# Performance work log

Measured on AMD Instinct MI355X. Metric: run time of the kernel, lower is better.

## Reference

```python
import jax, jax.numpy as jnp
import numpy as np

D_MODEL = 1024
D_STATE = 8
EXPAND = 2
EPS = 1e-5


def setup_inputs() -> dict:
    key = jax.random.key(0)
    ks = jax.random.split(key, 8)
    d_inner = D_MODEL * EXPAND
    x = jax.random.normal(ks[0], (2, 128, 196, D_MODEL), dtype=jnp.float32)
    # Linear params (torch convention: W [out, in], y = x @ W.T + b)
    W_proj = jax.random.normal(ks[1], (d_inner, D_MODEL), dtype=jnp.float32) * (1.0 / np.sqrt(D_MODEL))
    b_proj = jnp.zeros((d_inner,), dtype=jnp.float32)
    W_state = jax.random.normal(ks[2], (D_STATE, d_inner), dtype=jnp.float32) * (1.0 / np.sqrt(d_inner))
    b_state = jnp.zeros((D_STATE,), dtype=jnp.float32)
    W_out = jax.random.normal(ks[3], (D_MODEL, D_STATE), dtype=jnp.float32) * (1.0 / np.sqrt(D_STATE))
    b_out = jnp.zeros((D_MODEL,), dtype=jnp.float32)
    initial_state = jnp.zeros((1, D_STATE), dtype=jnp.float32)
    gamma = jnp.ones((D_MODEL,), dtype=jnp.float32)
    beta = jnp.zeros((D_MODEL,), dtype=jnp.float32)
    return {
        "x": x,
        "W_proj": W_proj, "b_proj": b_proj,
        "W_state": W_state, "b_state": b_state,
        "W_out": W_out, "b_out": b_out,
        "initial_state": initial_state,
        "gamma": gamma, "beta": beta,
    }


def reference(x, W_proj, b_proj, W_state, b_state, W_out, b_out, initial_state, gamma, beta):
    # The torch module loops over seq_len, but every step reads the fixed
    # initial_state (no recurrence) -> fully vectorized over all dims.
    # LayerNorm over d_model (eps=1e-5, torch default)
    mu = jnp.mean(x, axis=-1, keepdims=True)
    var = jnp.mean(jnp.square(x - mu), axis=-1, keepdims=True)
    xn = (x - mu) * jax.lax.rsqrt(var + EPS) * gamma + beta
    # proj: [b, s, p, d_model] -> [b, s, p, d_inner], then SiLU
    proj = jax.nn.silu(jnp.einsum('bspd,ed->bspe', xn, W_proj) + b_proj)
    # state projection: -> [b, s, p, d_state]
    state_updates = jnp.einsum('bspe,ne->bspn', proj, W_state) + b_state
    # initial_state [1, d_state] broadcast-added, then SiLU
    current_state = jax.nn.silu(initial_state.reshape(1, 1, 1, D_STATE) + state_updates)
    # out projection: -> [b, s, p, d_model]; dropout=0 (eval mode)
    out = jnp.einsum('bspn,dn->bspd', current_state, W_out) + b_out
    return x + out
```

## Files before the change

### kernel.cpp

```cpp
#include <hip/hip_runtime.h>
#include <hip/hip_bf16.h>

typedef unsigned short u16;
typedef unsigned int u32;
typedef __attribute__((ext_vector_type(8))) short bf16x8;
typedef __attribute__((ext_vector_type(4))) short bf16x4;
typedef __attribute__((ext_vector_type(8))) u16 u16x8;
typedef __attribute__((ext_vector_type(4))) float f32x4;

#define T_TOKENS 50176
#define D_MODEL  1024
#define D_INNER  2048
#define D_STATE  8

__device__ __forceinline__ u16 f2bf(float f) {
    u32 u = __builtin_bit_cast(u32, f);
    u += 0x7fffu + ((u >> 16) & 1u);
    return (u16)(u >> 16);
}
__device__ __forceinline__ float silu(float v) {
    return v / (1.f + __expf(-v));
}

__device__ __forceinline__ f32x4 mfma_16x16x16_bf16(bf16x4 a, bf16x4 b, f32x4 c) {
#if __has_builtin(__builtin_amdgcn_mfma_f32_16x16x16bf16_1k)
    return __builtin_amdgcn_mfma_f32_16x16x16bf16_1k(a, b, c, 0, 0, 0);
#else
    f32x4 d;
    asm("v_mfma_f32_16x16x16_bf16 %0, %1, %2, %3" : "=v"(d) : "v"(a), "v"(b), "v"(c));
    return d;
#endif
}

__global__ __launch_bounds__(256) void k_ln(const float* __restrict__ x,
                                            const float* __restrict__ gamma,
                                            const float* __restrict__ beta,
                                            u16* __restrict__ xn) {
    const int w = threadIdx.x >> 6, lane = threadIdx.x & 63;
    const int tok = blockIdx.x * 4 + w;
    const float* xr = x + (size_t)tok * D_MODEL;
    float4 v[2][2];
    float s1 = 0.f, s2 = 0.f;
#pragma unroll
    for (int c = 0; c < 2; ++c) {
        const int d = c * 512 + lane * 8;
        v[c][0] = *(const float4*)(xr + d);
        v[c][1] = *(const float4*)(xr + d + 4);
#pragma unroll
        for (int p = 0; p < 2; ++p) {
            s1 += v[c][p].x + v[c][p].y + v[c][p].z + v[c][p].w;
            s2 += v[c][p].x * v[c][p].x + v[c][p].y * v[c][p].y
                + v[c][p].z * v[c][p].z + v[c][p].w * v[c][p].w;
        }
    }
#pragma unroll
    for (int off = 32; off; off >>= 1) {
        s1 += __shfl_xor(s1, off, 64);
        s2 += __shfl_xor(s2, off, 64);
    }
    const float mu = s1 * (1.f / 1024.f);
    const float var = s2 * (1.f / 1024.f) - mu * mu;
    const float rstd = rsqrtf(var + 1e-5f);
    u16* orow = xn + (size_t)tok * D_MODEL;
#pragma unroll
    for (int c = 0; c < 2; ++c) {
        const int d = c * 512 + lane * 8;
        float4 g0 = *(const float4*)(gamma + d);
        float4 g1 = *(const float4*)(gamma + d + 4);
        float4 b0 = *(const float4*)(beta + d);
        float4 b1 = *(const float4*)(beta + d + 4);
        u16x8 o;
        o[0] = f2bf((v[c][0].x - mu) * rstd * g0.x + b0.x);
        o[1] = f2bf((v[c][0].y - mu) * rstd * g0.y + b0.y);
        o[2] = f2bf((v[c][0].z - mu) * rstd * g0.z + b0.z);
        o[3] = f2bf((v[c][0].w - mu) * rstd * g0.w + b0.w);
        o[4] = f2bf((v[c][1].x - mu) * rstd * g1.x + b1.x);
        o[5] = f2bf((v[c][1].y - mu) * rstd * g1.y + b1.y);
        o[6] = f2bf((v[c][1].z - mu) * rstd * g1.z + b1.z);
        o[7] = f2bf((v[c][1].w - mu) * rstd * g1.w + b1.w);
        *(u16x8*)(orow + d) = o;
    }
}

__global__ __launch_bounds__(256) void k_cvt(const float* __restrict__ W, u16* __restrict__ Wb) {
    const int i = (blockIdx.x * 256 + threadIdx.x) * 4;
    float4 v = *(const float4*)(W + i);
    ushort4 o = {f2bf(v.x), f2bf(v.y), f2bf(v.z), f2bf(v.w)};
    *(ushort4*)(Wb + i) = o;
}

#define STAGE_A(i, kb, buf) \
    __builtin_amdgcn_global_load_lds( \
        (const __attribute__((address_space(1))) void*)(Ag + (i) * 65536 + (kb) * 64), \
        (__attribute__((address_space(3))) void*)(lA + (buf) * 32768 + (i) * 4096), 16, 0, 0)
#define STAGE_B(i, kb, buf) \
    __builtin_amdgcn_global_load_lds( \
        (const __attribute__((address_space(1))) void*)(Bg + (i) * 65536 + (kb) * 64), \
        (__attribute__((address_space(3))) void*)(lB + (buf) * 32768 + (i) * 4096), 16, 0, 0)
#define FENCE() asm volatile("" ::: "memory")
#define BARRIER() do { FENCE(); __builtin_amdgcn_s_barrier(); FENCE(); } while (0)

__global__ __launch_bounds__(512, 2) void k_gemm(const u16* __restrict__ A,
                                                 const u16* __restrict__ B,
                                                 const float* __restrict__ bproj,
                                                 const float* __restrict__ Wstate,
                                                 float* __restrict__ part) {
    __shared__ u16 sm[65536];
    const int t = threadIdx.x;
    const int w = t >> 6, lane = t & 63;
    const int q = lane >> 4, c15 = lane & 15;
    const int bn = blockIdx.x, bm = blockIdx.y;
    const int wm = (w >> 2) * 128, wn = (w & 3) * 64;

    f32x4 acc[4][8];
#pragma unroll
    for (int ci = 0; ci < 4; ++ci)
#pragma unroll
        for (int ti = 0; ti < 8; ++ti) acc[ci][ti] = (f32x4){0.f, 0.f, 0.f, 0.f};

    const int srow = t >> 3;
    const int gch = (t & 7) ^ (srow & 7);
    const u16* Ag = A + (size_t)(bm * 256 + srow) * 1024 + gch * 8;
    const u16* Bg = B + (size_t)(bn * 256 + srow) * 1024 + gch * 8;
    u16* lA = &sm[t * 8];
    u16* lB = &sm[16384 + t * 8];

    auto LDA = [&](int buf, int ti, int ks) -> bf16x8 {
        const int row = wm + ti * 16 + c15;
        const int ch = (ks * 4 + q) ^ (c15 & 7);
        return *(const bf16x8*)&sm[buf * 32768 + row * 64 + ch * 8];
    };
    auto LDB = [&](int buf, int ci, int ks) -> bf16x8 {
        const int row = wn + ci * 16 + c15;
        const int ch = (ks * 4 + q) ^ (c15 & 7);
        return *(const bf16x8*)&sm[buf * 32768 + 16384 + row * 64 + ch * 8];
    };

    STAGE_A(0, 0, 0); STAGE_A(1, 0, 0); STAGE_A(2, 0, 0); STAGE_A(3, 0, 0);
    STAGE_B(0, 0, 0); STAGE_B(1, 0, 0); STAGE_B(2, 0, 0); STAGE_B(3, 0, 0);
    STAGE_A(0, 1, 1); STAGE_A(1, 1, 1);
    asm volatile("s_waitcnt vmcnt(2)" ::: "memory");
    BARRIER();

#pragma unroll 2
    for (int tt = 0; tt < 16; ++tt) {
        const int cur = tt & 1, nxt = cur ^ 1;
        const int kb1 = (tt + 1) & 15, kb2 = (tt + 2) & 15;
        bf16x8 xf[4][2], wf[4][2];
#pragma unroll
        for (int ti = 0; ti < 4; ++ti)
#pragma unroll
            for (int ks = 0; ks < 2; ++ks) xf[ti][ks] = LDA(cur, ti, ks);
#pragma unroll
        for (int ci = 0; ci < 2; ++ci)
#pragma unroll
            for (int ks = 0; ks < 2; ++ks) wf[ci][ks] = LDB(cur, ci, ks);
        STAGE_A(2, kb1, nxt); STAGE_A(3, kb1, nxt);
        BARRIER();
        __builtin_amdgcn_s_setprio(1);
#pragma unroll
        for (int ci = 0; ci < 2; ++ci)
#pragma unroll
            for (int ti = 0; ti < 4; ++ti)
#pragma unroll
                for (int ks = 0; ks < 2; ++ks)
                    acc[ci][ti] = __builtin_amdgcn_mfma_f32_16x16x32_bf16(wf[ci][ks], xf[ti][ks], acc[ci][ti], 0, 0, 0);
        __builtin_amdgcn_s_setprio(0);
        BARRIER();
#pragma unroll
        for (int ci = 2; ci < 4; ++ci)
#pragma unroll
            for (int ks = 0; ks < 2; ++ks) wf[ci][ks] = LDB(cur, ci, ks);
        STAGE_B(0, kb1, nxt); STAGE_B(1, kb1, nxt);
        BARRIER();
        __builtin_amdgcn_s_setprio(1);
#pragma unroll
        for (int ci = 2; ci < 4; ++ci)
#pragma unroll
            for (int ti = 0; ti < 4; ++ti)
#pragma unroll
                for (int ks = 0; ks < 2; ++ks)
                    acc[ci][ti] = __builtin_amdgcn_mfma_f32_16x16x32_bf16(wf[ci][ks], xf[ti][ks], acc[ci][ti], 0, 0, 0);
        __builtin_amdgcn_s_setprio(0);
        BARRIER();
#pragma unroll
        for (int ti = 0; ti < 4; ++ti)
#pragma unroll
            for (int ks = 0; ks < 2; ++ks) xf[ti][ks] = LDA(cur, 4 + ti, ks);
        STAGE_B(2, kb1, nxt); STAGE_B(3, kb1, nxt);
        BARRIER();
        __builtin_amdgcn_s_setprio(1);
#pragma unroll
        for (int ci = 0; ci < 2; ++ci)
#pragma unroll
            for (int ti = 0; ti < 4; ++ti)
#pragma unroll
                for (int ks = 0; ks < 2; ++ks)
                    acc[ci][4 + ti] = __builtin_amdgcn_mfma_f32_16x16x32_bf16(wf[ci][ks], xf[ti][ks], acc[ci][4 + ti], 0, 0, 0);
        __builtin_amdgcn_s_setprio(0);
        BARRIER();
        STAGE_A(0, kb2, cur); STAGE_A(1, kb2, cur);
        asm volatile("s_waitcnt vmcnt(2)" ::: "memory");
        BARRIER();
        __builtin_amdgcn_s_setprio(1);
#pragma unroll
        for (int ci = 2; ci < 4; ++ci)
#pragma unroll
            for (int ti = 0; ti < 4; ++ti)
#pragma unroll
                for (int ks = 0; ks < 2; ++ks)
                    acc[ci][4 + ti] = __builtin_amdgcn_mfma_f32_16x16x32_bf16(wf[ci][ks], xf[ti][ks], acc[ci][4 + ti], 0, 0, 0);
        __builtin_amdgcn_s_setprio(0);
        BARRIER();
    }

    const int ib0 = bn * 256 + wn + q * 4;
    f32x4 bp4[4];
    bf16x4 wsf[4];
#pragma unroll
    for (int ci = 0; ci < 4; ++ci) {
        const int ib = ib0 + ci * 16;
        bp4[ci] = *(const f32x4*)(bproj + ib);
        if (c15 < 8) {
            f32x4 wv = *(const f32x4*)(Wstate + (size_t)c15 * D_INNER + ib);
            wsf[ci] = (bf16x4){(short)f2bf(wv[0]), (short)f2bf(wv[1]), (short)f2bf(wv[2]), (short)f2bf(wv[3])};
        } else {
            wsf[ci] = (bf16x4){0, 0, 0, 0};
        }
    }
    const int slot = bn * 4 + (w & 3);
#pragma unroll
    for (int ti = 0; ti < 8; ++ti) {
        f32x4 a2 = (f32x4){0.f, 0.f, 0.f, 0.f};
#pragma unroll
        for (int ci = 0; ci < 4; ++ci) {
            bf16x4 sv;
#pragma unroll
            for (int r = 0; r < 4; ++r) {
                const float s = silu(acc[ci][ti][r] + bp4[ci][r]);
                sv[r] = (short)f2bf(s);
            }
            a2 = mfma_16x16x16_bf16(wsf[ci], sv, a2);
        }
        if (q < 2) {
            const int row = bm * 256 + wm + ti * 16 + c15;
            *(f32x4*)(part + (size_t)row * 256 + slot * 8 + q * 4) = a2;
        }
    }
}

__global__ __launch_bounds__(256) void k_out2(const float* __restrict__ x,
                                              const float* __restrict__ part,
                                              const float* __restrict__ Wout,
                                              const float* __restrict__ bout,
                                              const float* __restrict__ bstate,
                                              const float* __restrict__ s0,
                                              float* __restrict__ out) {
    __shared__ float wT[8][1024];
    const int t = threadIdx.x;
    const float4* Wg4 = (const float4*)Wout;
#pragma unroll
    for (int i = 0; i < 8; ++i) {
        const int g = i * 256 + t;
        const int d = g >> 1, h = (g & 1) * 4;
        float4 v = Wg4[g];
        wT[h + 0][d] = v.x;
        wT[h + 1][d] = v.y;
        wT[h + 2][d] = v.z;
        wT[h + 3][d] = v.w;
    }
    __syncthreads();

    const int w = t >> 6, lane = t & 63;
    const int tok = blockIdx.x * 4 + w;

    const float4* p4 = (const float4*)(part + (size_t)tok * 256);
    float4 pv = p4[lane];
    float pa[4] = {pv.x, pv.y, pv.z, pv.w};
#pragma unroll
    for (int off = 2; off < 64; off <<= 1)
#pragma unroll
        for (int j = 0; j < 4; ++j) pa[j] += __shfl_xor(pa[j], off, 64);
    float cs[8];
#pragma unroll
    for (int j = 0; j < 4; ++j) {
        const float sl = __shfl(pa[j], 0, 64);
        const float sh = __shfl(pa[j], 1, 64);
        cs[j]     = silu(sl + s0[j]     + bstate[j]);
        cs[4 + j] = silu(sh + s0[4 + j] + bstate[4 + j]);
    }

    const float4* xr4 = (const float4*)(x + (size_t)tok * D_MODEL);
    const float4* bo4 = (const float4*)bout;
    float4* o4 = (float4*)(out + (size_t)tok * D_MODEL);
#pragma unroll
    for (int c = 0; c < 4; ++c) {
        const int dv = c * 64 + lane;
        const int d = dv * 4;
        float4 xv = xr4[dv];
        float4 bv = bo4[dv];
        float4 r;
        r.x = xv.x + bv.x; r.y = xv.y + bv.y; r.z = xv.z + bv.z; r.w = xv.w + bv.w;
#pragma unroll
        for (int n = 0; n < 8; ++n) {
            const float4 wn = *(const float4*)&wT[n][d];
            r.x += cs[n] * wn.x;
            r.y += cs[n] * wn.y;
            r.z += cs[n] * wn.z;
            r.w += cs[n] * wn.w;
        }
        o4[dv] = r;
    }
}

extern "C" void kernel_launch(void* const* d_in, const int* in_sizes, int n_in,
                              void* d_out, int out_size, void* d_ws, size_t ws_size,
                              hipStream_t stream) {
    const float* x      = (const float*)d_in[0];
    const float* Wproj  = (const float*)d_in[1];
    const float* bproj  = (const float*)d_in[2];
    const float* Wstate = (const float*)d_in[3];
    const float* bstate = (const float*)d_in[4];
    const float* Wout   = (const float*)d_in[5];
    const float* bout   = (const float*)d_in[6];
    const float* s0     = (const float*)d_in[7];
    const float* gamma  = (const float*)d_in[8];
    const float* beta   = (const float*)d_in[9];

    u16* xn = (u16*)d_out;
    u16* Wb = (u16*)d_ws;
    float* partials = (float*)((char*)d_ws + (size_t)D_INNER * D_MODEL * sizeof(u16));
    float* out = (float*)d_out;

    k_ln  <<<T_TOKENS / 4, 256, 0, stream>>>(x, gamma, beta, xn);
    k_cvt <<<(D_INNER * D_MODEL) / 1024, 256, 0, stream>>>(Wproj, Wb);
    k_gemm<<<dim3(D_INNER / 256, T_TOKENS / 256), 512, 0, stream>>>(xn, Wb, bproj, Wstate, partials);
    k_out2<<<T_TOKENS / 4, 256, 0, stream>>>(x, partials, Wout, bout, bstate, s0, out);
}
```

Before: 680.1 us.

## Fuse weight convert into LN, reorder GEMM blocks, reduce partials in LDS

```diff
diff --git a/kernel.cpp b/kernel.cpp
--- a/kernel.cpp
+++ b/kernel.cpp
@@ -35,9 +35,19 @@
 __global__ __launch_bounds__(256) void k_ln(const float* __restrict__ x,
                                             const float* __restrict__ gamma,
                                             const float* __restrict__ beta,
-                                            u16* __restrict__ xn) {
+                                            u16* __restrict__ xn,
+                                            const float* __restrict__ W,
+                                            u16* __restrict__ Wb) {
+    const int bid = blockIdx.x;
+    if (bid >= 12544) {
+        const int i = ((bid - 12544) * 256 + threadIdx.x) * 4;
+        float4 v = *(const float4*)(W + i);
+        ushort4 o = {f2bf(v.x), f2bf(v.y), f2bf(v.z), f2bf(v.w)};
+        *(ushort4*)(Wb + i) = o;
+        return;
+    }
     const int w = threadIdx.x >> 6, lane = threadIdx.x & 63;
-    const int tok = blockIdx.x * 4 + w;
+    const int tok = bid * 4 + w;
     const float* xr = x + (size_t)tok * D_MODEL;
     float4 v[2][2];
     float s1 = 0.f, s2 = 0.f;
@@ -82,13 +92,6 @@
     }
 }
 
-__global__ __launch_bounds__(256) void k_cvt(const float* __restrict__ W, u16* __restrict__ Wb) {
-    const int i = (blockIdx.x * 256 + threadIdx.x) * 4;
-    float4 v = *(const float4*)(W + i);
-    ushort4 o = {f2bf(v.x), f2bf(v.y), f2bf(v.z), f2bf(v.w)};
-    *(ushort4*)(Wb + i) = o;
-}
-
 #define STAGE_A(i, kb, buf) \
     __builtin_amdgcn_global_load_lds( \
         (const __attribute__((address_space(1))) void*)(Ag + (i) * 65536 + (kb) * 64), \
@@ -109,7 +112,8 @@
     const int t = threadIdx.x;
     const int w = t >> 6, lane = t & 63;
     const int q = lane >> 4, c15 = lane & 15;
-    const int bn = blockIdx.x, bm = blockIdx.y;
+    const int lin = blockIdx.y * 8 + blockIdx.x;
+    const int bm = lin % 196, bn = lin / 196;
     const int wm = (w >> 2) * 128, wn = (w & 3) * 64;
 
     f32x4 acc[4][8];
@@ -214,6 +218,9 @@
         BARRIER();
     }
 
+    asm volatile("s_waitcnt vmcnt(0)" ::: "memory");
+    BARRIER();
+
     const int ib0 = bn * 256 + wn + q * 4;
     f32x4 bp4[4];
     bf16x4 wsf[4];
@@ -228,7 +235,8 @@
             wsf[ci] = (bf16x4){0, 0, 0, 0};
         }
     }
-    const int slot = bn * 4 + (w & 3);
+    float* smf = (float*)sm;
+    const int wq = w & 3;
 #pragma unroll
     for (int ti = 0; ti < 8; ++ti) {
         f32x4 a2 = (f32x4){0.f, 0.f, 0.f, 0.f};
@@ -243,9 +251,20 @@
             a2 = mfma_16x16x16_bf16(wsf[ci], sv, a2);
         }
         if (q < 2) {
-            const int row = bm * 256 + wm + ti * 16 + c15;
-            *(f32x4*)(part + (size_t)row * 256 + slot * 8 + q * 4) = a2;
-        }
+            const int tl = wm + ti * 16 + c15;
+            *(f32x4*)&smf[(wq * 256 + tl) * 8 + q * 4] = a2;
+        }
+    }
+    __syncthreads();
+    {
+        const int tl = t >> 1, s4 = (t & 1) * 4;
+        f32x4 s = (f32x4){0.f, 0.f, 0.f, 0.f};
+#pragma unroll
+        for (int sl = 0; sl < 4; ++sl) {
+            f32x4 v = *(const f32x4*)&smf[(sl * 256 + tl) * 8 + s4];
+            s[0] += v[0]; s[1] += v[1]; s[2] += v[2]; s[3] += v[3];
+        }
+        *(f32x4*)(part + (size_t)(bm * 256 + tl) * 64 + bn * 8 + s4) = s;
     }
 }
 
@@ -274,21 +293,14 @@
     const int w = t >> 6, lane = t & 63;
     const int tok = blockIdx.x * 4 + w;
 
-    const float4* p4 = (const float4*)(part + (size_t)tok * 256);
-    float4 pv = p4[lane];
-    float pa[4] = {pv.x, pv.y, pv.z, pv.w};
-#pragma unroll
-    for (int off = 2; off < 64; off <<= 1)
-#pragma unroll
-        for (int j = 0; j < 4; ++j) pa[j] += __shfl_xor(pa[j], off, 64);
+    float v = part[(size_t)tok * 64 + lane];
+#pragma unroll
+    for (int off = 8; off < 64; off <<= 1) v += __shfl_xor(v, off, 64);
+    const int st = lane & 7;
+    const float vv = silu(v + s0[st] + bstate[st]);
     float cs[8];
 #pragma unroll
-    for (int j = 0; j < 4; ++j) {
-        const float sl = __shfl(pa[j], 0, 64);
-        const float sh = __shfl(pa[j], 1, 64);
-        cs[j]     = silu(sl + s0[j]     + bstate[j]);
-        cs[4 + j] = silu(sh + s0[4 + j] + bstate[4 + j]);
-    }
+    for (int j = 0; j < 8; ++j) cs[j] = __shfl(vv, j, 64);
 
     const float4* xr4 = (const float4*)(x + (size_t)tok * D_MODEL);
     const float4* bo4 = (const float4*)bout;
@@ -332,8 +344,7 @@
     float* partials = (float*)((char*)d_ws + (size_t)D_INNER * D_MODEL * sizeof(u16));
     float* out = (float*)d_out;
 
-    k_ln  <<<T_TOKENS / 4, 256, 0, stream>>>(x, gamma, beta, xn);
-    k_cvt <<<(D_INNER * D_MODEL) / 1024, 256, 0, stream>>>(Wproj, Wb);
-    k_gemm<<<dim3(D_INNER / 256, T_TOKENS / 256), 512, 0, stream>>>(xn, Wb, bproj, Wstate, partials);
+    k_ln  <<<12544 + 2048, 256, 0, stream>>>(x, gamma, beta, xn, Wproj, Wb);
+    k_gemm<<<dim3(8, 196), 512, 0, stream>>>(xn, Wb, bproj, Wstate, partials);
     k_out2<<<T_TOKENS / 4, 256, 0, stream>>>(x, partials, Wout, bout, bstate, s0, out);
 }
```

Result: faster. 655.0 us (-3.7%).
